# Optimization experiments

Hardware: AMD Instinct MI355X
Metric: run time of the kernel (lower is better)

## Reference

```python
import math
import jax, jax.numpy as jnp
import numpy as np

DIM = 256
N_HEAD = 8
HEAD_SIZE = DIM // N_HEAD  # 32
B, N = 8, 2048


def setup_inputs() -> dict:
    key = jax.random.key(0)
    ks = jax.random.split(key, 6)
    return {
        "x": jax.random.normal(ks[0], (B, N, DIM), dtype=jnp.float32),
        "rel_pos": jax.random.uniform(ks[1], (B, N, N), dtype=jnp.float32),
        "W_qkv": jax.random.normal(ks[2], (3 * DIM, DIM), dtype=jnp.float32) * (1.0 / math.sqrt(DIM)),
        "b_qkv": jax.random.normal(ks[3], (3 * DIM,), dtype=jnp.float32) * 0.02,
        "W_d": jax.random.normal(ks[4], (DIM, 1), dtype=jnp.float32) * 0.02,
        "b_d": jax.random.normal(ks[5], (DIM,), dtype=jnp.float32) * 0.02,
    }


def reference(x, rel_pos, W_qkv, b_qkv, W_d, b_d):
    # degree gating: degree = sigmoid(Linear(1->dim)(rel_pos.sum(-1)))
    deg = jnp.sum(rel_pos, axis=-1, keepdims=True)            # [B, N, 1]
    gate = jax.nn.sigmoid(deg * W_d[:, 0] + b_d)              # [B, N, dim]
    x = x * gate

    qkv = jnp.einsum("bnd,ed->bne", x, W_qkv) + b_qkv          # [B, N, 3*dim]
    qk, value, res = jnp.split(qkv, 3, axis=-1)                # each [B, N, dim]
    qk = jax.nn.sigmoid(qk)

    scale = 1.0 / math.sqrt(HEAD_SIZE)
    attn = jnp.einsum("bnd,bmd->bnm", qk, qk) * scale          # [B, N, N]
    attn = attn * rel_pos                                      # elementwise rel_pos bias
    attn = attn / (jnp.sum(attn, axis=-1, keepdims=True) + 1e-6)  # row-sum normalization

    out = jax.nn.relu(jnp.einsum("bnm,bmd->bnd", attn, value) + res)
    return out
```

## Files before the change

### kernel.cpp

```cpp
#include <hip/hip_runtime.h>
#include <hip/hip_bf16.h>

#define NB 8
#define NN 2048
#define ND 256
#define SCALE 0.1767766952966369f

typedef __attribute__((ext_vector_type(8))) short short8;
typedef __attribute__((ext_vector_type(4))) float f32x4;
typedef unsigned short ushort_t;

static __device__ __forceinline__ ushort_t f2b(float f) {
    union { float f; unsigned int u; } v; v.f = f;
    unsigned int r = (v.u + 0x7FFFu + ((v.u >> 16) & 1u)) >> 16;
    return (ushort_t)r;
}

static __device__ __forceinline__ float sigmoidf_(float x) {
    return 1.0f / (1.0f + __expf(-x));
}

__global__ __launch_bounds__(256) void deggate_kernel(const float* __restrict__ rel,
                                                      const float* __restrict__ x,
                                                      const float* __restrict__ Wd,
                                                      const float* __restrict__ bd,
                                                      ushort_t* __restrict__ xg) {
    const int row = blockIdx.x;
    const int t = threadIdx.x;
    const float4* r4 = reinterpret_cast<const float4*>(rel + (size_t)row * NN);
    float4 a = r4[t * 2];
    float4 b = r4[t * 2 + 1];
    float s = a.x + a.y + a.z + a.w + b.x + b.y + b.z + b.w;
    for (int off = 1; off < 64; off <<= 1) s += __shfl_xor(s, off, 64);
    __shared__ float ws[4];
    if ((t & 63) == 0) ws[t >> 6] = s;
    __syncthreads();
    const float dg = ws[0] + ws[1] + ws[2] + ws[3];
    const float xv = x[(size_t)row * ND + t];
    xg[(size_t)row * ND + t] = f2b(xv * sigmoidf_(dg * Wd[t] + bd[t]));
}

__global__ __launch_bounds__(256) void wconv_kernel(const float* __restrict__ W,
                                                    ushort_t* __restrict__ Wb) {
    const int idx = (blockIdx.x * 256 + threadIdx.x) * 4;
    float4 wv = *reinterpret_cast<const float4*>(W + idx);
    ushort4 o;
    o.x = f2b(wv.x); o.y = f2b(wv.y); o.z = f2b(wv.z); o.w = f2b(wv.w);
    *reinterpret_cast<ushort4*>(Wb + idx) = o;
}

__global__ __launch_bounds__(256) void qkv_kernel(const ushort_t* __restrict__ xg,
                                                  const ushort_t* __restrict__ Wb,
                                                  const float* __restrict__ bqkv,
                                                  ushort_t* __restrict__ qk,
                                                  ushort_t* __restrict__ vT,
                                                  float* __restrict__ res) {
    __shared__ __align__(16) ushort_t T[64][72];
    const int t = threadIdx.x;
    const int w = t >> 6;
    const int l = t & 63;
    const int lr = l & 15;
    const int lg = l >> 4;
    const int n0 = blockIdx.x * 64 + w * 16;
    const int c0 = blockIdx.y * 64;

    f32x4 acc[4];
#pragma unroll
    for (int i = 0; i < 4; ++i) acc[i] = (f32x4){0.f, 0.f, 0.f, 0.f};

#pragma unroll
    for (int kb = 0; kb < 8; ++kb) {
        short8 a = *reinterpret_cast<const short8*>(xg + (size_t)(n0 + lr) * ND + kb * 32 + lg * 8);
#pragma unroll
        for (int ct = 0; ct < 4; ++ct) {
            short8 bb = *reinterpret_cast<const short8*>(Wb + (size_t)(c0 + ct * 16 + lr) * ND + kb * 32 + lg * 8);
            acc[ct] = __builtin_amdgcn_mfma_f32_16x16x32_bf16(a, bb, acc[ct], 0, 0, 0);
        }
    }

    if (blockIdx.y < 4) {
#pragma unroll
        for (int ct = 0; ct < 4; ++ct) {
            const int e = c0 + ct * 16 + lr;
            const float bias = bqkv[e];
#pragma unroll
            for (int r = 0; r < 4; ++r) {
                const int n = n0 + lg * 4 + r;
                qk[(size_t)n * ND + e] = f2b(sigmoidf_(acc[ct][r] + bias));
            }
        }
    } else if (blockIdx.y < 8) {
#pragma unroll
        for (int ct = 0; ct < 4; ++ct) {
            const int e = c0 + ct * 16 + lr;
            const float bias = bqkv[e];
#pragma unroll
            for (int r = 0; r < 4; ++r)
                T[ct * 16 + lr][w * 16 + lg * 4 + r] = f2b(acc[ct][r] + bias);
        }
        __syncthreads();
        const int e_loc = t >> 2;
        const int nl = (t & 3) * 16;
        const int d = c0 - 256 + e_loc;
        const int ng = blockIdx.x * 64;
        const int b = ng >> 11;
        size_t base = ((size_t)b * ND + d) * NN + (ng & 2047) + nl;
        *reinterpret_cast<short8*>(vT + base)     = *reinterpret_cast<const short8*>(&T[e_loc][nl]);
        *reinterpret_cast<short8*>(vT + base + 8) = *reinterpret_cast<const short8*>(&T[e_loc][nl + 8]);
    } else {
#pragma unroll
        for (int ct = 0; ct < 4; ++ct) {
            const int e = c0 + ct * 16 + lr;
            const float bias = bqkv[e];
#pragma unroll
            for (int r = 0; r < 4; ++r) {
                const int n = n0 + lg * 4 + r;
                res[(size_t)n * ND + (e - 512)] = acc[ct][r] + bias;
            }
        }
    }
}

__global__ __launch_bounds__(256, 4) void attn_kernel(const ushort_t* __restrict__ qk,
                                                      const ushort_t* __restrict__ vT,
                                                      const float* __restrict__ rel,
                                                      const float* __restrict__ res,
                                                      float* __restrict__ out) {
    __shared__ __align__(16) ushort_t slds[2][16][144];
    __shared__ float dsums[4][16];
    const int t = threadIdx.x;
    const int w = t >> 6;
    const int l = t & 63;
    const int lr = l & 15;
    const int lg = l >> 4;
    const int b = blockIdx.y;
    const int q0 = blockIdx.x * 16;

    const ushort_t* qkb = qk + (size_t)b * NN * ND;
    const ushort_t* vTb = vT + (size_t)b * ND * NN;
    const float* relb = rel + (size_t)b * NN * NN;

    short8 aq[8];
#pragma unroll
    for (int kb = 0; kb < 8; ++kb)
        aq[kb] = *reinterpret_cast<const short8*>(qkb + (size_t)(q0 + lr) * ND + kb * 32 + lg * 8);

    f32x4 acc[4];
#pragma unroll
    for (int i = 0; i < 4; ++i) acc[i] = (f32x4){0.f, 0.f, 0.f, 0.f};
    float dsum[4] = {0.f, 0.f, 0.f, 0.f};

    for (int mt = 0; mt < 16; ++mt) {
        const int m0 = mt * 128;
        const int mw = m0 + w * 32;
        const int buf = mt & 1;

        float rp0[4], rp1[4];
#pragma unroll
        for (int r = 0; r < 4; ++r) {
            const int qrow = q0 + lg * 4 + r;
            rp0[r] = relb[(size_t)qrow * NN + mw + lr];
            rp1[r] = relb[(size_t)qrow * NN + mw + 16 + lr];
        }

        f32x4 s0 = (f32x4){0.f, 0.f, 0.f, 0.f};
        f32x4 s1 = (f32x4){0.f, 0.f, 0.f, 0.f};
#pragma unroll
        for (int kb = 0; kb < 8; ++kb) {
            short8 b0 = *reinterpret_cast<const short8*>(qkb + (size_t)(mw + lr) * ND + kb * 32 + lg * 8);
            short8 b1 = *reinterpret_cast<const short8*>(qkb + (size_t)(mw + 16 + lr) * ND + kb * 32 + lg * 8);
            s0 = __builtin_amdgcn_mfma_f32_16x16x32_bf16(aq[kb], b0, s0, 0, 0, 0);
            s1 = __builtin_amdgcn_mfma_f32_16x16x32_bf16(aq[kb], b1, s1, 0, 0, 0);
        }

#pragma unroll
        for (int r = 0; r < 4; ++r) {
            float v0 = s0[r] * SCALE * rp0[r];
            float v1 = s1[r] * SCALE * rp1[r];
            dsum[r] += v0 + v1;
            slds[buf][lg * 4 + r][w * 32 + lr] = f2b(v0);
            slds[buf][lg * 4 + r][w * 32 + 16 + lr] = f2b(v1);
        }
        __syncthreads();

        short8 pa[4];
#pragma unroll
        for (int kt = 0; kt < 4; ++kt)
            pa[kt] = *reinterpret_cast<const short8*>(&slds[buf][lr][kt * 32 + lg * 8]);
#pragma unroll
        for (int dt = 0; dt < 4; ++dt) {
#pragma unroll
            for (int kt = 0; kt < 4; ++kt) {
                short8 bv = *reinterpret_cast<const short8*>(
                    vTb + (size_t)(w * 64 + dt * 16 + lr) * NN + m0 + kt * 32 + lg * 8);
                acc[dt] = __builtin_amdgcn_mfma_f32_16x16x32_bf16(pa[kt], bv, acc[dt], 0, 0, 0);
            }
        }
    }

#pragma unroll
    for (int r = 0; r < 4; ++r) {
        float v = dsum[r];
        v += __shfl_xor(v, 1, 64);
        v += __shfl_xor(v, 2, 64);
        v += __shfl_xor(v, 4, 64);
        v += __shfl_xor(v, 8, 64);
        dsum[r] = v;
    }
    __syncthreads();
    if (lr == 0) {
#pragma unroll
        for (int r = 0; r < 4; ++r) dsums[w][lg * 4 + r] = dsum[r];
    }
    __syncthreads();
    float inv[4];
#pragma unroll
    for (int r = 0; r < 4; ++r) {
        const int q = lg * 4 + r;
        float tot = dsums[0][q] + dsums[1][q] + dsums[2][q] + dsums[3][q];
        inv[r] = 1.0f / (tot + 1e-6f);
    }

#pragma unroll
    for (int dt = 0; dt < 4; ++dt) {
#pragma unroll
        for (int r = 0; r < 4; ++r) {
            const size_t o = ((size_t)b * NN + q0 + lg * 4 + r) * ND + w * 64 + dt * 16 + lr;
            float v = acc[dt][r] * inv[r] + res[o];
            out[o] = fmaxf(v, 0.f);
        }
    }
}

extern "C" void kernel_launch(void* const* d_in, const int* in_sizes, int n_in,
                              void* d_out, int out_size, void* d_ws, size_t ws_size,
                              hipStream_t stream) {
    const float* x    = (const float*)d_in[0];
    const float* rel  = (const float*)d_in[1];
    const float* Wqkv = (const float*)d_in[2];
    const float* bqkv = (const float*)d_in[3];
    const float* Wd   = (const float*)d_in[4];
    const float* bd   = (const float*)d_in[5];
    float* out = (float*)d_out;

    char* ws = (char*)d_ws;
    ushort_t* Wb  = (ushort_t*)(ws + 0);
    ushort_t* xg  = (ushort_t*)(ws + 0x80000);
    ushort_t* qkb = (ushort_t*)(ws + 0x880000);
    ushort_t* vT  = (ushort_t*)(ws + 0x1080000);
    float*    res = (float*)(ws + 0x1880000);

    deggate_kernel<<<NB * NN, 256, 0, stream>>>(rel, x, Wd, bd, xg);
    wconv_kernel<<<(3 * ND * ND) / 1024, 256, 0, stream>>>(Wqkv, Wb);
    qkv_kernel<<<dim3(NB * NN / 64, 12), 256, 0, stream>>>(xg, Wb, bqkv, qkb, vT, res);
    attn_kernel<<<dim3(NN / 16, NB), 256, 0, stream>>>(qkb, vT, rel, res, out);
}
```

Baseline: 502.7 us.

## Use 8 waves per attention block and prefetch rel_pos tiles one step ahead

The attention kernel now runs 512 threads (8 waves) per block. Each outer step covers 256 keys instead of 128, and each wave owns 32 output columns instead of 64, which halves the accumulator registers per wave. The rel_pos values for the next key tile are loaded into registers one iteration ahead to hide global load latency. The wider block raises the LDS tile size and the per-step synchronisation cost across more waves, and the launch-bounds occupancy hint is changed.

```diff
diff --git a/kernel.cpp b/kernel.cpp
--- a/kernel.cpp
+++ b/kernel.cpp
@@ -121,13 +121,13 @@
     }
 }
 
-__global__ __launch_bounds__(256, 4) void attn_kernel(const ushort_t* __restrict__ qk,
+__global__ __launch_bounds__(512, 6) void attn_kernel(const ushort_t* __restrict__ qk,
                                                       const ushort_t* __restrict__ vT,
                                                       const float* __restrict__ rel,
                                                       const float* __restrict__ res,
                                                       float* __restrict__ out) {
-    __shared__ __align__(16) ushort_t slds[2][16][144];
-    __shared__ float dsums[4][16];
+    __shared__ __align__(16) ushort_t slds[2][16][264];
+    __shared__ float dsums[8][16];
     const int t = threadIdx.x;
     const int w = t >> 6;
     const int l = t & 63;
@@ -145,30 +145,43 @@
     for (int kb = 0; kb < 8; ++kb)
         aq[kb] = *reinterpret_cast<const short8*>(qkb + (size_t)(q0 + lr) * ND + kb * 32 + lg * 8);
 
-    f32x4 acc[4];
-#pragma unroll
-    for (int i = 0; i < 4; ++i) acc[i] = (f32x4){0.f, 0.f, 0.f, 0.f};
+    f32x4 acc0 = (f32x4){0.f, 0.f, 0.f, 0.f};
+    f32x4 acc1 = (f32x4){0.f, 0.f, 0.f, 0.f};
     float dsum[4] = {0.f, 0.f, 0.f, 0.f};
 
-    for (int mt = 0; mt < 16; ++mt) {
-        const int m0 = mt * 128;
-        const int mw = m0 + w * 32;
+    float rpa[4], rpb[4];
+#pragma unroll
+    for (int r = 0; r < 4; ++r) {
+        const size_t rb = (size_t)(q0 + lg * 4 + r) * NN + w * 32;
+        rpa[r] = relb[rb + lr];
+        rpb[r] = relb[rb + 16 + lr];
+    }
+
+#pragma unroll 2
+    for (int mt = 0; mt < 8; ++mt) {
+        const int m0 = mt * 256;
+        const int mwv = m0 + w * 32;
         const int buf = mt & 1;
 
         float rp0[4], rp1[4];
 #pragma unroll
-        for (int r = 0; r < 4; ++r) {
-            const int qrow = q0 + lg * 4 + r;
-            rp0[r] = relb[(size_t)qrow * NN + mw + lr];
-            rp1[r] = relb[(size_t)qrow * NN + mw + 16 + lr];
+        for (int r = 0; r < 4; ++r) { rp0[r] = rpa[r]; rp1[r] = rpb[r]; }
+        if (mt < 7) {
+            const int mn = (mt + 1) * 256 + w * 32;
+#pragma unroll
+            for (int r = 0; r < 4; ++r) {
+                const size_t rb = (size_t)(q0 + lg * 4 + r) * NN + mn;
+                rpa[r] = relb[rb + lr];
+                rpb[r] = relb[rb + 16 + lr];
+            }
         }
 
         f32x4 s0 = (f32x4){0.f, 0.f, 0.f, 0.f};
         f32x4 s1 = (f32x4){0.f, 0.f, 0.f, 0.f};
 #pragma unroll
         for (int kb = 0; kb < 8; ++kb) {
-            short8 b0 = *reinterpret_cast<const short8*>(qkb + (size_t)(mw + lr) * ND + kb * 32 + lg * 8);
-            short8 b1 = *reinterpret_cast<const short8*>(qkb + (size_t)(mw + 16 + lr) * ND + kb * 32 + lg * 8);
+            short8 b0 = *reinterpret_cast<const short8*>(qkb + (size_t)(mwv + lr) * ND + kb * 32 + lg * 8);
+            short8 b1 = *reinterpret_cast<const short8*>(qkb + (size_t)(mwv + 16 + lr) * ND + kb * 32 + lg * 8);
             s0 = __builtin_amdgcn_mfma_f32_16x16x32_bf16(aq[kb], b0, s0, 0, 0, 0);
             s1 = __builtin_amdgcn_mfma_f32_16x16x32_bf16(aq[kb], b1, s1, 0, 0, 0);
         }
@@ -183,18 +196,15 @@
         }
         __syncthreads();
 
-        short8 pa[4];
-#pragma unroll
-        for (int kt = 0; kt < 4; ++kt)
-            pa[kt] = *reinterpret_cast<const short8*>(&slds[buf][lr][kt * 32 + lg * 8]);
-#pragma unroll
-        for (int dt = 0; dt < 4; ++dt) {
-#pragma unroll
-            for (int kt = 0; kt < 4; ++kt) {
-                short8 bv = *reinterpret_cast<const short8*>(
-                    vTb + (size_t)(w * 64 + dt * 16 + lr) * NN + m0 + kt * 32 + lg * 8);
-                acc[dt] = __builtin_amdgcn_mfma_f32_16x16x32_bf16(pa[kt], bv, acc[dt], 0, 0, 0);
-            }
+#pragma unroll
+        for (int kt = 0; kt < 8; ++kt) {
+            short8 pa = *reinterpret_cast<const short8*>(&slds[buf][lr][kt * 32 + lg * 8]);
+            short8 bv0 = *reinterpret_cast<const short8*>(
+                vTb + (size_t)(w * 32 + lr) * NN + m0 + kt * 32 + lg * 8);
+            short8 bv1 = *reinterpret_cast<const short8*>(
+                vTb + (size_t)(w * 32 + 16 + lr) * NN + m0 + kt * 32 + lg * 8);
+            acc0 = __builtin_amdgcn_mfma_f32_16x16x32_bf16(pa, bv0, acc0, 0, 0, 0);
+            acc1 = __builtin_amdgcn_mfma_f32_16x16x32_bf16(pa, bv1, acc1, 0, 0, 0);
         }
     }
 
@@ -217,18 +227,19 @@
 #pragma unroll
     for (int r = 0; r < 4; ++r) {
         const int q = lg * 4 + r;
-        float tot = dsums[0][q] + dsums[1][q] + dsums[2][q] + dsums[3][q];
+        float tot = 0.f;
+#pragma unroll
+        for (int ww = 0; ww < 8; ++ww) tot += dsums[ww][q];
         inv[r] = 1.0f / (tot + 1e-6f);
     }
 
 #pragma unroll
-    for (int dt = 0; dt < 4; ++dt) {
-#pragma unroll
-        for (int r = 0; r < 4; ++r) {
-            const size_t o = ((size_t)b * NN + q0 + lg * 4 + r) * ND + w * 64 + dt * 16 + lr;
-            float v = acc[dt][r] * inv[r] + res[o];
-            out[o] = fmaxf(v, 0.f);
-        }
+    for (int r = 0; r < 4; ++r) {
+        const size_t o = ((size_t)b * NN + q0 + lg * 4 + r) * ND + w * 32 + lr;
+        float v0 = acc0[r] * inv[r] + res[o];
+        float v1 = acc1[r] * inv[r] + res[o + 16];
+        out[o] = fmaxf(v0, 0.f);
+        out[o + 16] = fmaxf(v1, 0.f);
     }
 }
 
@@ -253,5 +264,5 @@
     deggate_kernel<<<NB * NN, 256, 0, stream>>>(rel, x, Wd, bd, xg);
     wconv_kernel<<<(3 * ND * ND) / 1024, 256, 0, stream>>>(Wqkv, Wb);
     qkv_kernel<<<dim3(NB * NN / 64, 12), 256, 0, stream>>>(xg, Wb, bqkv, qkb, vT, res);
-    attn_kernel<<<dim3(NN / 16, NB), 256, 0, stream>>>(qkb, vT, rel, res, out);
-}
+    attn_kernel<<<dim3(NN / 16, NB), 512, 0, stream>>>(qkb, vT, rel, res, out);
+}
```

Result: slower. 580.9 us (+15.6%).
